# Performance work log

Hardware: AMD Instinct MI355X
Metric: run time of the kernel (lower is better)

## Reference

```python
import jax, jax.numpy as jnp
import numpy as np

D, ED, N, R, K, NL = 128, 256, 16, 8, 4, 3   # d_model, d_inner, d_state, dt_rank, d_conv, n_layers
B, L = 4, 1024
HID, OUT = 256, 2
EPS = 1e-5


def setup_inputs() -> dict:
    key = jax.random.key(0)
    ks = jax.random.split(key, 16)
    g = lambda k, shape, s=0.05: jax.random.normal(k, shape, dtype=jnp.float32) * s
    return {
        "x": jax.random.normal(ks[0], (B, L, D), dtype=jnp.float32),
        # Mamba params, stacked over (2 directions, NL layers)
        "rms_w": jnp.ones((2, NL, D), jnp.float32),
        "in_w": g(ks[1], (2, NL, 2 * ED, D)),
        "in_b": g(ks[2], (2, NL, 2 * ED)),
        "conv_w": g(ks[3], (2, NL, ED, K)),
        "conv_b": g(ks[4], (2, NL, ED)),
        "xproj_w": g(ks[5], (2, NL, R + 2 * N, ED)),
        "dt_w": g(ks[6], (2, NL, ED, R)),
        "dt_b": g(ks[7], (2, NL, ED)),
        "A_log": jnp.broadcast_to(jnp.log(jnp.arange(1.0, N + 1.0, dtype=jnp.float32)), (2, NL, ED, N)) + 0.0,
        "Dp": jnp.ones((2, NL, ED), jnp.float32),
        "out_w": g(ks[8], (2, NL, D, ED)),
        "out_b": g(ks[9], (2, NL, D)),
        # MLP head params (BatchNorm in training mode: batch stats)
        "bn1_g": jnp.ones((2 * D,), jnp.float32), "bn1_b": jnp.zeros((2 * D,), jnp.float32),
        "w1": g(ks[10], (HID, 2 * D)), "b1": g(ks[11], (HID,)),
        "bn2_g": jnp.ones((HID,), jnp.float32), "bn2_b": jnp.zeros((HID,), jnp.float32),
        "w2": g(ks[12], (HID, HID)), "b2": g(ks[13], (HID,)),
        "bn3_g": jnp.ones((HID,), jnp.float32), "bn3_b": jnp.zeros((HID,), jnp.float32),
        "w3": g(ks[14], (OUT, HID)), "b3": g(ks[15], (OUT,)),
    }


def _rms(x, w):
    return x * jax.lax.rsqrt(jnp.mean(x * x, axis=-1, keepdims=True) + EPS) * w


def _dwconv(x, w, b):
    # causal depthwise conv; x: (B,L,ED), w: (ED,K)
    y = jax.lax.conv_general_dilated(x.transpose(0, 2, 1), w[:, None, :], (1,), [(K - 1, 0)],
                                     feature_group_count=ED, dimension_numbers=("NCH", "OIH", "NCH"))
    return y.transpose(0, 2, 1) + b


def _ssm(dA, dBx, C):
    # dA,dBx: (B,L,ED,N); C: (B,L,N) -> y: (B,L,ED)
    def step(h, inp):
        a, bx, c = inp
        h = a * h + bx
        return h, jnp.einsum("ben,bn->be", h, c)
    h0 = jnp.zeros((dA.shape[0], ED, N), dA.dtype)
    _, ys = jax.lax.scan(step, h0, (dA.transpose(1, 0, 2, 3), dBx.transpose(1, 0, 2, 3), C.transpose(1, 0, 2)))
    return ys.transpose(1, 0, 2)


def _block(x, in_w, in_b, conv_w, conv_b, xproj_w, dt_w, dt_b, A_log, Dp, out_w, out_b):
    xz = x @ in_w.T + in_b
    xi, z = xz[..., :ED], xz[..., ED:]
    xi = jax.nn.silu(_dwconv(xi, conv_w, conv_b))
    dbc = xi @ xproj_w.T
    dt, Bm, Cm = dbc[..., :R], dbc[..., R:R + N], dbc[..., R + N:]
    delta = jax.nn.softplus(dt @ dt_w.T + dt_b)            # (B,L,ED)
    A = -jnp.exp(A_log)                                    # (ED,N)
    dA = jnp.exp(delta[..., None] * A)                     # (B,L,ED,N)
    dBx = (delta * xi)[..., None] * Bm[:, :, None, :]      # (B,L,ED,N)
    y = _ssm(dA, dBx, Cm) + Dp * xi
    y = y * jax.nn.silu(z)
    return y @ out_w.T + out_b


def _mamba(x, d, rms_w, in_w, in_b, conv_w, conv_b, xproj_w, dt_w, dt_b, A_log, Dp, out_w, out_b):
    for l in range(NL):
        x = x + _block(_rms(x, rms_w[d, l]), in_w[d, l], in_b[d, l], conv_w[d, l], conv_b[d, l],
                       xproj_w[d, l], dt_w[d, l], dt_b[d, l], A_log[d, l], Dp[d, l], out_w[d, l], out_b[d, l])
    return x


def _bn(x, g, b):
    m = jnp.mean(x, axis=0)
    v = jnp.mean((x - m) ** 2, axis=0)  # biased var, torch BN training mode
    return (x - m) * jax.lax.rsqrt(v + EPS) * g + b


def _forward(x, rms_w, in_w, in_b, conv_w, conv_b, xproj_w, dt_w, dt_b, A_log, Dp, out_w, out_b,
             bn1_g, bn1_b, w1, b1, bn2_g, bn2_b, w2, b2, bn3_g, bn3_b, w3, b3):
    mp = (rms_w, in_w, in_b, conv_w, conv_b, xproj_w, dt_w, dt_b, A_log, Dp, out_w, out_b)
    fwd = _mamba(x, 0, *mp)
    bwd = jnp.flip(_mamba(jnp.flip(x, axis=1), 1, *mp), axis=1)
    h = jnp.concatenate([fwd, bwd], axis=2).reshape(B * L, 2 * D)
    h = jax.nn.leaky_relu(_bn(h, bn1_g, bn1_b) @ w1.T + b1)
    h = jax.nn.leaky_relu(_bn(h, bn2_g, bn2_b) @ w2.T + b2)
    h = _bn(h, bn3_g, bn3_b) @ w3.T + b3
    return h.reshape(B, L, OUT)


def reference(x, rms_w, in_w, in_b, conv_w, conv_b, xproj_w, dt_w, dt_b, A_log, Dp, out_w, out_b,
              bn1_g, bn1_b, w1, b1, bn2_g, bn2_b, w2, b2, bn3_g, bn3_b, w3, b3):
    return _forward(x, rms_w, in_w, in_b, conv_w, conv_b, xproj_w, dt_w, dt_b, A_log, Dp, out_w, out_b,
                    bn1_g, bn1_b, w1, b1, bn2_g, bn2_b, w2, b2, bn3_g, bn3_b, w3, b3)
```

## Files before the change

### kernel.cpp

```cpp
#include <hip/hip_runtime.h>
#include <hip/hip_bf16.h>
#include <hip/hip_fp16.h>

#define NL 3
#define EPS 1e-5f

#define C_INB    393984L
#define C_CONVW  397056L
#define C_CONVB  403200L
#define C_XPROJW 404736L
#define C_DTW    466176L
#define C_DTB    478464L
#define C_ALOG   480000L
#define C_DP     504576L
#define C_OUTB   702720L
#define C_BN1G   703488L
#define C_BN1B   703744L
#define C_B1     769536L
#define C_BN2G   769792L
#define C_BN2B   770048L
#define C_B2     835840L
#define C_BN3G   836096L
#define C_BN3B   836352L
#define C_W3     836608L
#define C_B3     837120L
#define FLAG_OFF 837184L
#define X0_OFF   837248L
#define X1_OFF   1361536L
#define XZT_OFF  1885824L
#define DBCT_OFF 8177280L
#define YGP_OFF  8504960L
#define BNA_OFF  10603648L
#define HINW_OFF  10605184L
#define HOUTW_OFF 10801792L
#define HW1_OFF   10900096L
#define HW2_OFF   10932864L
#define H1_OFF   XZT_OFF
#define H2_OFF   (XZT_OFF + 1048576L)

#define ASLD 68

struct Ptrs { const void* p[25]; };

typedef _Float16 half8 __attribute__((ext_vector_type(8)));
typedef float f32x4 __attribute__((ext_vector_type(4)));

static __device__ const int  CV_SRC[21] = {0,0,3,4,5,6,7,8,9,10,12,13,14,16,17,18,20,21,22,23,24};
static __device__ const long CV_DST[21] = {X0_OFF,X1_OFF,C_INB,C_CONVW,C_CONVB,C_XPROJW,C_DTW,C_DTB,C_ALOG,C_DP,
                                           C_OUTB,C_BN1G,C_BN1B,C_B1,C_BN2G,C_BN2B,C_B2,C_BN3G,C_BN3B,C_W3,C_B3};
static __device__ const int  CV_SZ[21]  = {524288,524288,3072,6144,1536,61440,12288,1536,24576,1536,
                                           768,256,256,256,256,256,256,256,256,512,2};

__device__ inline float ldsrc(const void* s, long i, bool isbf) {
  if (isbf) { unsigned int u = ((const unsigned short*)s)[i]; return __uint_as_float(u << 16); }
  return ((const float*)s)[i];
}

__global__ __launch_bounds__(256) void g_convert(Ptrs ps, float* __restrict__ ws) {
  bool isbf = (*(const unsigned int*)ps.p[1]) == 0x3F803F80u;
  int job = blockIdx.y;
  if (job == 0 && blockIdx.x == 0 && threadIdx.x == 0) ws[FLAG_OFF] = isbf ? 1.f : 0.f;
  int tid0 = blockIdx.x * 256 + threadIdx.x;
  int stride = gridDim.x * 256;
  if (job < 21) {
    int n = CV_SZ[job];
    const void* s = ps.p[CV_SRC[job]];
    float* dp = ws + CV_DST[job];
    bool permute = (job < 2);
    for (int i = tid0; i < n; i += stride) {
      long si = i;
      if (permute) {
        int row = i >> 7, col = i & 127;
        int b = row >> 10, p = row & 1023;
        int t = ((p & 63) << 4) + (p >> 6);
        si = ((long)((b << 10) + t) << 7) + col;
      }
      dp[i] = ldsrc(s, si, isbf);
    }
  } else if (job == 21) {
    _Float16* dp = (_Float16*)(ws + HINW_OFF);
    const void* sw = ps.p[2]; const void* sr = ps.p[1];
    for (int i = tid0; i < 393216; i += stride) {
      int dl = i >> 16, k = i & 127;
      float v = ldsrc(sw, i, isbf) * ldsrc(sr, dl*128 + k, isbf);
      dp[i] = (_Float16)v;
    }
  } else if (job == 22) {
    _Float16* dp = (_Float16*)(ws + HOUTW_OFF);
    const void* s = ps.p[11];
    for (int i = tid0; i < 196608; i += stride) dp[i] = (_Float16)ldsrc(s, i, isbf);
  } else if (job == 23) {
    _Float16* dp = (_Float16*)(ws + HW1_OFF);
    const void* s = ps.p[15];
    for (int i = tid0; i < 65536; i += stride) dp[i] = (_Float16)ldsrc(s, i, isbf);
  } else if (job == 24) {
    _Float16* dp = (_Float16*)(ws + HW2_OFF);
    const void* s = ps.p[19];
    for (int i = tid0; i < 65536; i += stride) dp[i] = (_Float16)ldsrc(s, i, isbf);
  } else {
    for (int i = tid0; i < 1536; i += stride) ws[BNA_OFF + i] = 0.f;
  }
}

__device__ inline void mm_inner(const float* As, const float* Bs, float4* acc) {
  int tx = threadIdx.x & 15, ty = threadIdx.x >> 4;
  #pragma unroll
  for (int k = 0; k < 64; ++k) {
    float4 av = *(const float4*)&As[k*ASLD + ty*4];
    float4 bv = *(const float4*)&Bs[k*ASLD + tx*4];
    acc[0].x = fmaf(av.x,bv.x,acc[0].x); acc[0].y = fmaf(av.x,bv.y,acc[0].y); acc[0].z = fmaf(av.x,bv.z,acc[0].z); acc[0].w = fmaf(av.x,bv.w,acc[0].w);
    acc[1].x = fmaf(av.y,bv.x,acc[1].x); acc[1].y = fmaf(av.y,bv.y,acc[1].y); acc[1].z = fmaf(av.y,bv.z,acc[1].z); acc[1].w = fmaf(av.y,bv.w,acc[1].w);
    acc[2].x = fmaf(av.z,bv.x,acc[2].x); acc[2].y = fmaf(av.z,bv.y,acc[2].y); acc[2].z = fmaf(av.z,bv.z,acc[2].z); acc[2].w = fmaf(av.z,bv.w,acc[2].w);
    acc[3].x = fmaf(av.w,bv.x,acc[3].x); acc[3].y = fmaf(av.w,bv.y,acc[3].y); acc[3].z = fmaf(av.w,bv.z,acc[3].z); acc[3].w = fmaf(av.w,bv.w,acc[3].w);
  }
}

__device__ inline void stageT_g(float* S, const float* src, int ld, int row0, int k0, int nvalid) {
  int m = threadIdx.x >> 2, q = threadIdx.x & 3;
  const float* p = src + (long)(row0 + m) * ld + k0 + q*16;
  bool ok = (row0 + m) < nvalid;
  #pragma unroll
  for (int j = 0; j < 4; ++j) {
    float4 v = ok ? *(const float4*)(p + j*4) : make_float4(0.f,0.f,0.f,0.f);
    int kk = q*16 + j*4;
    S[(kk+0)*ASLD+m] = v.x; S[(kk+1)*ASLD+m] = v.y; S[(kk+2)*ASLD+m] = v.z; S[(kk+3)*ASLD+m] = v.w;
  }
}

__device__ inline float softplusf(float x) {
  if (x > 20.f) return x;
  return __logf(1.f + __expf(x));
}
__device__ inline float siluf(float a) { return a / (1.f + __expf(-a)); }

__global__ __launch_bounds__(256) void g_k1m(float* __restrict__ ws, int layer) {
  int d = blockIdx.z, nt = blockIdx.y, pt = blockIdx.x;
  const float* X = ws + (d ? X1_OFF : X0_OFF);
  const _Float16* Wf = (const _Float16*)(ws + HINW_OFF) + (long)(d*NL+layer)*65536;
  const float* Bi = ws + C_INB + (d*NL+layer)*512;
  __shared__ float rsq[256];
  __shared__ float rsc[64];
  int p0 = pt*64;
  {
    int row = threadIdx.x >> 2, q = threadIdx.x & 3;
    const float* xp = X + (long)(p0+row)*128 + q*32;
    float s = 0.f;
    #pragma unroll
    for (int j = 0; j < 8; ++j) {
      float4 v = *(const float4*)(xp + j*4);
      s += v.x*v.x + v.y*v.y + v.z*v.z + v.w*v.w;
    }
    rsq[row*4+q] = s;
  }
  __syncthreads();
  if (threadIdx.x < 64) {
    float s = rsq[threadIdx.x*4] + rsq[threadIdx.x*4+1] + rsq[threadIdx.x*4+2] + rsq[threadIdx.x*4+3];
    rsc[threadIdx.x] = rsqrtf(s * (1.f/128.f) + EPS);
  }
  __syncthreads();
  int w = threadIdx.x >> 6, lane = threadIdx.x & 63;
  int quad = lane >> 4, lm = lane & 15;
  int n0 = nt*64 + w*16;
  f32x4 zero = {0.f,0.f,0.f,0.f};
  f32x4 acc[4] = {zero, zero, zero, zero};
  #pragma unroll
  for (int s = 0; s < 4; ++s) {
    int k0 = s*32 + quad*8;
    half8 af = *(const half8*)(Wf + (long)(n0+lm)*128 + k0);
    #pragma unroll
    for (int t = 0; t < 4; ++t) {
      int pr = t*16 + lm;
      const float* xp = X + (long)(p0+pr)*128 + k0;
      float4 v0 = *(const float4*)xp;
      float4 v1 = *(const float4*)(xp+4);
      float r = rsc[pr];
      half8 bf;
      bf[0]=(_Float16)(v0.x*r); bf[1]=(_Float16)(v0.y*r); bf[2]=(_Float16)(v0.z*r); bf[3]=(_Float16)(v0.w*r);
      bf[4]=(_Float16)(v1.x*r); bf[5]=(_Float16)(v1.y*r); bf[6]=(_Float16)(v1.z*r); bf[7]=(_Float16)(v1.w*r);
      acc[t] = __builtin_amdgcn_mfma_f32_16x16x32_f16(af, bf, acc[t], 0, 0, 0);
    }
  }
  float* xzt = ws + XZT_OFF + (long)d*2097152L;
  #pragma unroll
  for (int r = 0; r < 4; ++r) {
    int n = n0 + quad*4 + r;
    float bias = Bi[n];
    #pragma unroll
    for (int t = 0; t < 4; ++t) {
      int p = p0 + t*16 + lm;
      xzt[(long)n*4096 + p] = acc[t][r] + bias;
    }
  }
}

__global__ __launch_bounds__(256) void g_k3c(float* __restrict__ ws, int layer) {
  int d = blockIdx.z, mt = blockIdx.x;
  int m0 = mt * 64;
  int bb = mt >> 4, ii = mt & 15;
  const float* xzbase = ws + XZT_OFF + (long)d*2097152L;
  const float* W = ws + C_XPROJW + (long)((d*NL+layer)*40) * 256;
  const float* cw = ws + C_CONVW + (long)(d*NL+layer)*1024;
  const float* cbp = ws + C_CONVB + (d*NL+layer)*256;
  __shared__ float As[64*ASLD];
  __shared__ float Bs[64*ASLD];
  int colb[4]; int edge[4];
  #pragma unroll
  for (int j = 0; j < 4; ++j) {
    if (d == 0) {
      int iq = ii - j;
      if (iq >= 0) { colb[j] = iq*64; edge[j] = 0; }
      else         { colb[j] = (iq+16)*64 - 1; edge[j] = 1; }
    } else {
      int iq = ii + j;
      if (iq <= 15) { colb[j] = iq*64; edge[j] = 0; }
      else          { colb[j] = (iq-16)*64 + 1; edge[j] = 2; }
    }
  }
  int m = threadIdx.x & 63, er = threadIdx.x >> 6;
  float4 acc[4] = {make_float4(0,0,0,0),make_float4(0,0,0,0),make_float4(0,0,0,0),make_float4(0,0,0,0)};
  for (int kt = 0; kt < 4; ++kt) {
    for (int pass = 0; pass < 16; ++pass) {
      int el = pass*4 + er;
      int e = kt*64 + el;
      const float* xr = xzbase + (long)e*4096 + bb*1024;
      float4 cwv = *(const float4*)(cw + e*4);
      float cb = cbp[e];
      float xv[4];
      #pragma unroll
      for (int j = 0; j < 4; ++j) {
        bool msk = (edge[j] == 1 && m == 0) || (edge[j] == 2 && m == 63);
        xv[j] = msk ? 0.f : xr[colb[j] + m];
      }
      float a = cb + cwv.w*xv[0] + cwv.z*xv[1] + cwv.y*xv[2] + cwv.x*xv[3];
      As[el*ASLD + m] = siluf(a);
    }
    stageT_g(Bs, W, 256, 0, kt*64, 40);
    __syncthreads();
    mm_inner(As, Bs, acc);
    __syncthreads();
  }
  int tx = threadIdx.x & 15, ty = threadIdx.x >> 4;
  #pragma unroll
  for (int i = 0; i < 4; ++i) {
    const float* av = (const float*)&acc[i];
    #pragma unroll
    for (int cc = 0; cc < 4; ++cc) {
      Bs[(tx*4+cc)*65 + ty*4+i] = av[cc];
    }
  }
  __syncthreads();
  float* dbcT = ws + DBCT_OFF + (long)d*163840L;
  #pragma unroll
  for (int r = 0; r < 10; ++r) {
    int el = r*256 + threadIdx.x;
    int n = el >> 6, mm = el & 63;
    dbcT[(long)n*4096 + m0 + mm] = Bs[n*65 + mm];
  }
}

__global__ __launch_bounds__(256) void g_k5c(float* __restrict__ ws, int layer) {
  int d = blockIdx.z, b = blockIdx.y, eg = blockIdx.x;
  int es = threadIdx.x >> 6;
  int c  = threadIdx.x & 63;
  int e = eg*4 + es;
  int g0 = b*1024 + c;
  const float* xzrow = ws + XZT_OFF + (long)d*2097152L + (long)e*4096 + g0;
  const float* zp    = ws + XZT_OFF + (long)d*2097152L + (long)(256+e)*4096 + g0;
  const float* dbc = ws + DBCT_OFF + (long)d*163840L + g0;
  float*       yo  = ws + YGP_OFF + (long)d*1048576L + (long)e*4096 + g0;
  const float* dw = ws + C_DTW + (long)((d*NL+layer)*256 + e)*8;
  float dtb = ws[C_DTB + (d*NL+layer)*256 + e];
  const float* al = ws + C_ALOG + (long)((d*NL+layer)*256 + e)*16;
  float Dpe = ws[C_DP + (d*NL+layer)*256 + e];
  float4 cwv = *(const float4*)(ws + C_CONVW + (long)((d*NL+layer)*256 + e)*4);
  float cb = ws[C_CONVB + (d*NL+layer)*256 + e];
  float dtw[8];
  #pragma unroll
  for (int n = 0; n < 8; ++n) dtw[n] = dw[n];
  float Anv[16]; bool fast = true;
  #pragma unroll
  for (int n = 0; n < 16; ++n) {
    Anv[n] = -__expf(al[n]);
    fast = fast && (fabsf(Anv[n] + (float)(n+1)) < 1e-3f * (float)(n+1));
  }
  float w1, w2, w3;
  if (d == 0) {
    if (c > 0) { w1 = xzrow[959]; w2 = xzrow[895]; w3 = xzrow[831]; }
    else { w1 = w2 = w3 = 0.f; }
  } else {
    if (c < 63) { w1 = xzrow[1]; w2 = xzrow[65]; w3 = xzrow[129]; }
    else { w1 = w2 = w3 = 0.f; }
  }
  __shared__ float aL[4*64*17];
  __shared__ float hL[4*64*17];
  float h[16], ap[16], del[16], xcv[16];
  float Q = 1.f;
  #pragma unroll
  for (int n = 0; n < 16; ++n) { h[n] = 0.f; ap[n] = 1.f; }
  int i0 = d ? 15 : 0, di = d ? -1 : 1;
  for (int s = 0; s < 16; ++s) {
    int i = i0 + s*di;
    int off = i*64;
    float a0 = dtb;
    #pragma unroll
    for (int n = 0; n < 8; ++n) a0 += dbc[(long)n*4096 + off] * dtw[n];
    float dl = softplusf(a0);
    float xt = xzrow[off];
    float xc = siluf(cb + cwv.w*xt + cwv.z*w1 + cwv.y*w2 + cwv.x*w3);
    w3 = w2; w2 = w1; w1 = xt;
    del[s] = dl; xcv[s] = xc;
    float dx = dl * xc;
    if (fast) {
      float q = __expf(-dl);
      float qp[16];
      qp[0]=q; qp[1]=q*q; qp[2]=qp[1]*q; qp[3]=qp[1]*qp[1];
      float q4=qp[3];
      qp[4]=qp[0]*q4; qp[5]=qp[1]*q4; qp[6]=qp[2]*q4; qp[7]=q4*q4;
      float q8=qp[7];
      #pragma unroll
      for (int j = 0; j < 8; ++j) qp[8+j]=qp[j]*q8;
      Q *= q;
      #pragma unroll
      for (int n = 0; n < 16; ++n)
        h[n] = fmaf(qp[n], h[n], dx * dbc[(long)(8+n)*4096 + off]);
    } else {
      #pragma unroll
      for (int n = 0; n < 16; ++n) {
        float a = __expf(dl * Anv[n]);
        ap[n] *= a;
        h[n] = fmaf(a, h[n], dx * dbc[(long)(8+n)*4096 + off]);
      }
    }
  }
  if (fast) {
    float p = Q;
    #pragma unroll
    for (int n = 0; n < 16; ++n) { ap[n] = p; p *= Q; }
  }
  int base = (es*64 + c)*17;
  #pragma unroll
  for (int n = 0; n < 16; ++n) { aL[base+n] = ap[n]; hL[base+n] = h[n]; }
  __syncthreads();
  if (threadIdx.x < 64) {
    int e2 = threadIdx.x >> 4, n = threadIdx.x & 15;
    float h0 = 0.f;
    for (int s2 = 0; s2 < 64; ++s2) {
      int cc = d ? (63 - s2) : s2;
      int ix = (e2*64 + cc)*17 + n;
      float ta = aL[ix], th = hL[ix];
      aL[ix] = h0;
      h0 = fmaf(ta, h0, th);
    }
  }
  __syncthreads();
  #pragma unroll
  for (int n = 0; n < 16; ++n) h[n] = aL[base+n];
  for (int s = 0; s < 16; ++s) {
    int i = i0 + s*di;
    int off = i*64;
    float dl = del[s], xc = xcv[s];
    float dx = dl * xc;
    float zr = zp[off];
    float zg = zr / (1.f + __expf(-zr));
    float ya[4] = {0.f,0.f,0.f,0.f};
    if (fast) {
      float q = __expf(-dl);
      float qp[16];
      qp[0]=q; qp[1]=q*q; qp[2]=qp[1]*q; qp[3]=qp[1]*qp[1];
      float q4=qp[3];
      qp[4]=qp[0]*q4; qp[5]=qp[1]*q4; qp[6]=qp[2]*q4; qp[7]=q4*q4;
      float q8=qp[7];
      #pragma unroll
      for (int j = 0; j < 8; ++j) qp[8+j]=qp[j]*q8;
      #pragma unroll
      for (int n = 0; n < 16; ++n) {
        h[n] = fmaf(qp[n], h[n], dx * dbc[(long)(8+n)*4096 + off]);
        ya[n & 3] = fmaf(h[n], dbc[(long)(24+n)*4096 + off], ya[n & 3]);
      }
    } else {
      #pragma unroll
      for (int n = 0; n < 16; ++n) {
        float a = __expf(dl * Anv[n]);
        h[n] = fmaf(a, h[n], dx * dbc[(long)(8+n)*4096 + off]);
        ya[n & 3] = fmaf(h[n], dbc[(long)(24+n)*4096 + off], ya[n & 3]);
      }
    }
    float y = (ya[0] + ya[1]) + (ya[2] + ya[3]);
    y = fmaf(Dpe, xc, y);
    yo[off] = y * zg;
  }
}

__global__ __launch_bounds__(256) void g_k61(float* __restrict__ ws, int layer) {
  int d = blockIdx.z, pt = blockIdx.x;
  int p0 = pt*16;
  const float* Y = ws + YGP_OFF + (long)d*1048576L;
  const _Float16* Wf = (const _Float16*)(ws + HOUTW_OFF) + (long)(d*NL+layer)*32768;
  const float* Ob = ws + C_OUTB + (d*NL+layer)*128;
  float* Xd = ws + (d ? X1_OFF : X0_OFF);
  __shared__ __align__(16) _Float16 Ah[16*264];
  __shared__ float Xn[16*137];
  __shared__ float rsq[64];
  __shared__ float rsc[16];
  {
    int e = threadIdx.x;
    const float* yp = Y + (long)e*4096 + p0;
    float4 v0 = *(const float4*)yp;
    float4 v1 = *(const float4*)(yp+4);
    float4 v2 = *(const float4*)(yp+8);
    float4 v3 = *(const float4*)(yp+12);
    float vv[16] = {v0.x,v0.y,v0.z,v0.w, v1.x,v1.y,v1.z,v1.w,
                    v2.x,v2.y,v2.z,v2.w, v3.x,v3.y,v3.z,v3.w};
    #pragma unroll
    for (int p = 0; p < 16; ++p) Ah[p*264 + e] = (_Float16)vv[p];
  }
  __syncthreads();
  int w = threadIdx.x >> 6, lane = threadIdx.x & 63;
  int quad = lane >> 4, lm = lane & 15;
  f32x4 zero = {0.f,0.f,0.f,0.f};
  f32x4 acc[2] = {zero, zero};
  #pragma unroll
  for (int s = 0; s < 8; ++s) {
    int k0 = s*32 + quad*8;
    half8 af = *(const half8*)(&Ah[lm*264 + k0]);
    #pragma unroll
    for (int t = 0; t < 2; ++t) {
      int n = w*32 + t*16 + lm;
      half8 bf = *(const half8*)(Wf + (long)n*256 + k0);
      acc[t] = __builtin_amdgcn_mfma_f32_16x16x32_f16(af, bf, acc[t], 0, 0, 0);
    }
  }
  bool dostats = (layer == NL-1);
  float* bna = ws + BNA_OFF;
  #pragma unroll
  for (int t = 0; t < 2; ++t) {
    int n = w*32 + t*16 + lm;
    float ob = Ob[n];
    float s1 = 0.f, s2 = 0.f;
    #pragma unroll
    for (int r = 0; r < 4; ++r) {
      int p = p0 + quad*4 + r;
      float v = acc[t][r] + ob + Xd[(long)p*128 + n];
      Xd[(long)p*128 + n] = v;
      Xn[(quad*4 + r)*137 + n] = v;
      s1 += v; s2 += v*v;
    }
    if (dostats) {
      s1 += __shfl_xor(s1, 16, 64); s2 += __shfl_xor(s2, 16, 64);
      s1 += __shfl_xor(s1, 32, 64); s2 += __shfl_xor(s2, 32, 64);
      if (quad == 0) {
        int ch = d*128 + n;
        atomicAdd(&bna[ch], s1);
        atomicAdd(&bna[256 + ch], s2);
      }
    }
  }
  if (layer == NL-1) return;
  __syncthreads();
  if (threadIdx.x < 64) {
    int pl = threadIdx.x >> 2, qq = threadIdx.x & 3;
    float s = 0.f;
    const float* xr = &Xn[pl*137 + qq*32];
    #pragma unroll
    for (int k = 0; k < 32; ++k) s += xr[k]*xr[k];
    rsq[threadIdx.x] = s;
  }
  __syncthreads();
  if (threadIdx.x < 16) {
    float s = rsq[threadIdx.x*4] + rsq[threadIdx.x*4+1] + rsq[threadIdx.x*4+2] + rsq[threadIdx.x*4+3];
    rsc[threadIdx.x] = rsqrtf(s * (1.f/128.f) + EPS);
  }
  __syncthreads();
  const _Float16* Wn = (const _Float16*)(ws + HINW_OFF) + (long)(d*NL+layer+1)*65536;
  const float* Bi = ws + C_INB + (d*NL+layer+1)*512;
  f32x4 acc2[8] = {zero,zero,zero,zero,zero,zero,zero,zero};
  float r = rsc[lm];
  #pragma unroll
  for (int s = 0; s < 4; ++s) {
    int k0 = s*32 + quad*8;
    half8 bf;
    const float* xr = &Xn[lm*137 + k0];
    #pragma unroll
    for (int j = 0; j < 8; ++j) bf[j] = (_Float16)(xr[j] * r);
    #pragma unroll
    for (int tt = 0; tt < 8; ++tt) {
      int n2 = w*128 + tt*16 + lm;
      half8 af = *(const half8*)(Wn + (long)n2*128 + k0);
      acc2[tt] = __builtin_amdgcn_mfma_f32_16x16x32_f16(af, bf, acc2[tt], 0, 0, 0);
    }
  }
  float* xzt = ws + XZT_OFF + (long)d*2097152L;
  #pragma unroll
  for (int tt = 0; tt < 8; ++tt) {
    #pragma unroll
    for (int rr = 0; rr < 4; ++rr) {
      int n2 = w*128 + tt*16 + quad*4 + rr;
      xzt[(long)n2*4096 + p0 + lm] = acc2[tt][rr] + Bi[n2];
    }
  }
}

template<int STAGE>
__global__ __launch_bounds__(256) void g_hgm(float* __restrict__ ws) {
  int p0 = blockIdx.x * 16;
  __shared__ float scL[256], shL[256];
  {
    int k = threadIdx.x;
    float S = ws[BNA_OFF + STAGE*512 + k], S2 = ws[BNA_OFF + STAGE*512 + 256 + k];
    float mean = S * (1.f/4096.f);
    float var = S2 * (1.f/4096.f) - mean*mean;
    const float* g = ws + (STAGE == 0 ? C_BN1G : C_BN2G);
    const float* bb = ws + (STAGE == 0 ? C_BN1B : C_BN2B);
    float sc = g[k] * rsqrtf(var + EPS);
    scL[k] = sc; shL[k] = bb[k] - mean*sc;
  }
  __syncthreads();
  const _Float16* Wf = (const _Float16*)(ws + (STAGE == 0 ? HW1_OFF : HW2_OFF));
  const float* bias = ws + (STAGE == 0 ? C_B1 : C_B2);
  float* H = ws + (STAGE == 0 ? H1_OFF : H2_OFF);
  int w = threadIdx.x >> 6, lane = threadIdx.x & 63;
  int quad = lane >> 4, lm = lane & 15;
  f32x4 zero = {0.f,0.f,0.f,0.f};
  f32x4 acc[4] = {zero, zero, zero, zero};
  #pragma unroll
  for (int s = 0; s < 8; ++s) {
    int k0 = s*32 + quad*8;
    const float* src;
    if (STAGE == 0) src = (k0 < 128) ? (ws + X0_OFF + (long)(p0+lm)*128 + k0)
                                     : (ws + X1_OFF + (long)(p0+lm)*128 + (k0-128));
    else            src = ws + H1_OFF + (long)(p0+lm)*256 + k0;
    float4 v0 = *(const float4*)src, v1 = *(const float4*)(src+4);
    float4 c0 = *(const float4*)&scL[k0], c1 = *(const float4*)&scL[k0+4];
    float4 h0 = *(const float4*)&shL[k0], h1 = *(const float4*)&shL[k0+4];
    half8 af;
    af[0]=(_Float16)(v0.x*c0.x+h0.x); af[1]=(_Float16)(v0.y*c0.y+h0.y);
    af[2]=(_Float16)(v0.z*c0.z+h0.z); af[3]=(_Float16)(v0.w*c0.w+h0.w);
    af[4]=(_Float16)(v1.x*c1.x+h1.x); af[5]=(_Float16)(v1.y*c1.y+h1.y);
    af[6]=(_Float16)(v1.z*c1.z+h1.z); af[7]=(_Float16)(v1.w*c1.w+h1.w);
    #pragma unroll
    for (int t = 0; t < 4; ++t) {
      int n = w*64 + t*16 + lm;
      half8 bf = *(const half8*)(Wf + (long)n*256 + k0);
      acc[t] = __builtin_amdgcn_mfma_f32_16x16x32_f16(af, bf, acc[t], 0, 0, 0);
    }
  }
  float* bna = ws + BNA_OFF + (STAGE+1)*512;
  #pragma unroll
  for (int t = 0; t < 4; ++t) {
    int n = w*64 + t*16 + lm;
    float bs = bias[n];
    float s1 = 0.f, s2 = 0.f;
    #pragma unroll
    for (int r = 0; r < 4; ++r) {
      int p = p0 + quad*4 + r;
      float v = acc[t][r] + bs;
      v = v > 0.f ? v : 0.01f*v;
      H[(long)p*256 + n] = v;
      s1 += v; s2 += v*v;
    }
    s1 += __shfl_xor(s1, 16, 64); s2 += __shfl_xor(s2, 16, 64);
    s1 += __shfl_xor(s1, 32, 64); s2 += __shfl_xor(s2, 32, 64);
    if (quad == 0) {
      atomicAdd(&bna[n], s1);
      atomicAdd(&bna[256 + n], s2);
    }
  }
}

__global__ __launch_bounds__(256) void g_hg2(float* __restrict__ ws, void* dout) {
  int mt = blockIdx.x;
  __shared__ float As[64*ASLD];
  __shared__ float Bs[64*ASLD];
  __shared__ float scL[256], shL[256];
  {
    int k = threadIdx.x;
    float S = ws[BNA_OFF + 2*512 + k], S2 = ws[BNA_OFF + 2*512 + 256 + k];
    float mean = S * (1.f/4096.f);
    float var = S2 * (1.f/4096.f) - mean*mean;
    float sc = ws[C_BN3G + k] * rsqrtf(var + EPS);
    scL[k] = sc; shL[k] = ws[C_BN3B + k] - mean*sc;
  }
  __syncthreads();
  float4 acc[4] = {make_float4(0,0,0,0),make_float4(0,0,0,0),make_float4(0,0,0,0),make_float4(0,0,0,0)};
  for (int kt = 0; kt < 4; ++kt) {
    int k0 = kt * 64;
    {
      int m = threadIdx.x >> 2, q = threadIdx.x & 3;
      const float* p = ws + H2_OFF + (long)(mt*64 + m)*256 + k0 + q*16;
      #pragma unroll
      for (int j = 0; j < 4; ++j) {
        float4 v  = *(const float4*)(p + j*4);
        float4 s4 = *(const float4*)&scL[k0 + q*16 + j*4];
        float4 h4 = *(const float4*)&shL[k0 + q*16 + j*4];
        int kk = q*16 + j*4;
        As[(kk+0)*ASLD+m] = v.x*s4.x + h4.x; As[(kk+1)*ASLD+m] = v.y*s4.y + h4.y;
        As[(kk+2)*ASLD+m] = v.z*s4.z + h4.z; As[(kk+3)*ASLD+m] = v.w*s4.w + h4.w;
      }
    }
    stageT_g(Bs, ws + C_W3, 256, 0, k0, 2);
    __syncthreads();
    mm_inner(As, Bs, acc);
    __syncthreads();
  }
  int tx = threadIdx.x & 15, ty = threadIdx.x >> 4;
  if (tx == 0) {
    bool isbf = ws[FLAG_OFF] != 0.f;
    float b0 = ws[C_B3], b1 = ws[C_B3 + 1];
    #pragma unroll
    for (int i = 0; i < 4; ++i) {
      int r = mt*64 + ty*4 + i;
      int b = r >> 10, p = r & 1023;
      int t = ((p & 63) << 4) + (p >> 6);
      long tok = (long)(b << 10) + t;
      float v0 = acc[i].x + b0, v1 = acc[i].y + b1;
      if (isbf) {
        __hip_bfloat16* o = (__hip_bfloat16*)dout;
        o[tok*2]   = __float2bfloat16(v0);
        o[tok*2+1] = __float2bfloat16(v1);
      } else {
        float* o = (float*)dout;
        o[tok*2] = v0; o[tok*2+1] = v1;
      }
    }
  }
}

extern "C" void kernel_launch(void* const* d_in, const int* in_sizes, int n_in,
                              void* d_out, int out_size, void* d_ws, size_t ws_size,
                              hipStream_t stream) {
  (void)in_sizes; (void)n_in; (void)out_size; (void)ws_size;
  float* ws = (float*)d_ws;
  Ptrs ps;
  for (int i = 0; i < 25; ++i) ps.p[i] = d_in[i];
  g_convert<<<dim3(32, 26), dim3(256), 0, stream>>>(ps, ws);
  g_k1m<<<dim3(64, 8, 2), dim3(256), 0, stream>>>(ws, 0);
  for (int l = 0; l < NL; ++l) {
    g_k3c<<<dim3(64, 1, 2), dim3(256), 0, stream>>>(ws, l);
    g_k5c<<<dim3(64, 4, 2), dim3(256), 0, stream>>>(ws, l);
    g_k61<<<dim3(256, 1, 2), dim3(256), 0, stream>>>(ws, l);
  }
  g_hgm<0><<<dim3(256), dim3(256), 0, stream>>>(ws);
  g_hgm<1><<<dim3(256), dim3(256), 0, stream>>>(ws);
  g_hg2<<<dim3(64), dim3(256), 0, stream>>>(ws, d_out);
}
```

Baseline: 468.7 us.

## Use fp16 MFMA for conv+x_proj kernel with pre-converted padded weights

Replaces the fp32 SIMT-tiled conv+SiLU+x_proj kernel with one that stages the activated conv output as fp16 in shared memory and multiplies it against fp16 x_proj weights using 16x16x32 MFMA instructions. The weights are converted once in the setup kernel, padded from 40 to 64 rows and stored in a new workspace region. The grid moves from 128 blocks of 64 tokens to 256 blocks of 32 tokens. The aim is to cut FMA time and raise parallelism, at the cost of fp16 rounding on the x_proj inputs and some wasted work on the padded rows.

Result: faster. 405.2 us (-13.6%).

```diff
diff --git a/kernel.cpp b/kernel.cpp
--- a/kernel.cpp
+++ b/kernel.cpp
@@ -35,6 +35,7 @@
 #define HOUTW_OFF 10801792L
 #define HW1_OFF   10900096L
 #define HW2_OFF   10932864L
+#define HXW_OFF   10965632L
 #define H1_OFF   XZT_OFF
 #define H2_OFF   (XZT_OFF + 1048576L)
 
@@ -97,8 +98,18 @@
     _Float16* dp = (_Float16*)(ws + HW2_OFF);
     const void* s = ps.p[19];
     for (int i = tid0; i < 65536; i += stride) dp[i] = (_Float16)ldsrc(s, i, isbf);
+  } else if (job == 25) {
+    for (int i = tid0; i < 1536; i += stride) ws[BNA_OFF + i] = 0.f;
   } else {
-    for (int i = tid0; i < 1536; i += stride) ws[BNA_OFF + i] = 0.f;
+    _Float16* dp = (_Float16*)(ws + HXW_OFF);
+    const void* s = ps.p[5];
+    for (int i = tid0; i < 98304; i += stride) {
+      int dl = i >> 14;
+      int rem = i & 16383;
+      int nn = rem >> 8, k = rem & 255;
+      float v = (nn < 40) ? ldsrc(s, (long)(dl*40+nn)*256 + k, isbf) : 0.f;
+      dp[i] = (_Float16)v;
+    }
   }
 }
 
@@ -193,68 +204,70 @@
   }
 }
 
-__global__ __launch_bounds__(256) void g_k3c(float* __restrict__ ws, int layer) {
-  int d = blockIdx.z, mt = blockIdx.x;
-  int m0 = mt * 64;
-  int bb = mt >> 4, ii = mt & 15;
-  const float* xzbase = ws + XZT_OFF + (long)d*2097152L;
-  const float* W = ws + C_XPROJW + (long)((d*NL+layer)*40) * 256;
+#define AHLD 264
+__global__ __launch_bounds__(256) void g_k3m(float* __restrict__ ws, int layer) {
+  int d = blockIdx.z, b = blockIdx.y;
+  int ii = blockIdx.x >> 1, c0 = (blockIdx.x & 1) * 32;
+  const float* xz = ws + XZT_OFF + (long)d*2097152L;
   const float* cw = ws + C_CONVW + (long)(d*NL+layer)*1024;
   const float* cbp = ws + C_CONVB + (d*NL+layer)*256;
-  __shared__ float As[64*ASLD];
-  __shared__ float Bs[64*ASLD];
-  int colb[4]; int edge[4];
-  #pragma unroll
-  for (int j = 0; j < 4; ++j) {
-    if (d == 0) {
-      int iq = ii - j;
-      if (iq >= 0) { colb[j] = iq*64; edge[j] = 0; }
-      else         { colb[j] = (iq+16)*64 - 1; edge[j] = 1; }
-    } else {
-      int iq = ii + j;
-      if (iq <= 15) { colb[j] = iq*64; edge[j] = 0; }
-      else          { colb[j] = (iq-16)*64 + 1; edge[j] = 2; }
-    }
-  }
-  int m = threadIdx.x & 63, er = threadIdx.x >> 6;
-  float4 acc[4] = {make_float4(0,0,0,0),make_float4(0,0,0,0),make_float4(0,0,0,0),make_float4(0,0,0,0)};
-  for (int kt = 0; kt < 4; ++kt) {
-    for (int pass = 0; pass < 16; ++pass) {
-      int el = pass*4 + er;
-      int e = kt*64 + el;
-      const float* xr = xzbase + (long)e*4096 + bb*1024;
-      float4 cwv = *(const float4*)(cw + e*4);
-      float cb = cbp[e];
-      float xv[4];
-      #pragma unroll
-      for (int j = 0; j < 4; ++j) {
-        bool msk = (edge[j] == 1 && m == 0) || (edge[j] == 2 && m == 63);
-        xv[j] = msk ? 0.f : xr[colb[j] + m];
-      }
-      float a = cb + cwv.w*xv[0] + cwv.z*xv[1] + cwv.y*xv[2] + cwv.x*xv[3];
-      As[el*ASLD + m] = siluf(a);
-    }
-    stageT_g(Bs, W, 256, 0, kt*64, 40);
-    __syncthreads();
-    mm_inner(As, Bs, acc);
-    __syncthreads();
-  }
-  int tx = threadIdx.x & 15, ty = threadIdx.x >> 4;
-  #pragma unroll
-  for (int i = 0; i < 4; ++i) {
-    const float* av = (const float*)&acc[i];
-    #pragma unroll
-    for (int cc = 0; cc < 4; ++cc) {
-      Bs[(tx*4+cc)*65 + ty*4+i] = av[cc];
-    }
-  }
-  __syncthreads();
+  const _Float16* Wx = (const _Float16*)(ws + HXW_OFF) + (long)(d*NL+layer)*16384;
+  __shared__ __align__(16) _Float16 Ah[32*AHLD];
+  int col[4], sh[4];
+  col[0] = ii; sh[0] = 0;
+  #pragma unroll
+  for (int j = 1; j < 4; ++j) {
+    if (d == 0) { if (ii-j >= 0) { col[j]=ii-j; sh[j]=0; } else { col[j]=ii-j+16; sh[j]=-1; } }
+    else        { if (ii+j <= 15){ col[j]=ii+j; sh[j]=0; } else { col[j]=ii+j-16; sh[j]=1; } }
+  }
+  int c = threadIdx.x & 31, eh = threadIdx.x >> 5;
+  int gc = c0 + c;
+  long rowbase = (long)b*1024;
+  for (int r = 0; r < 32; ++r) {
+    int e = eh*32 + r;
+    const float* xrow = xz + (long)e*4096 + rowbase;
+    float4 cwv = *(const float4*)(cw + e*4);
+    float v0 = xrow[col[0]*64 + gc];
+    float v1, v2, v3;
+    {
+      bool bad = (sh[1] < 0 && gc == 0) || (sh[1] > 0 && gc == 63);
+      v1 = bad ? 0.f : xrow[col[1]*64 + gc + sh[1]];
+    }
+    {
+      bool bad = (sh[2] < 0 && gc == 0) || (sh[2] > 0 && gc == 63);
+      v2 = bad ? 0.f : xrow[col[2]*64 + gc + sh[2]];
+    }
+    {
+      bool bad = (sh[3] < 0 && gc == 0) || (sh[3] > 0 && gc == 63);
+      v3 = bad ? 0.f : xrow[col[3]*64 + gc + sh[3]];
+    }
+    float a = cbp[e] + cwv.w*v0 + cwv.z*v1 + cwv.y*v2 + cwv.x*v3;
+    Ah[c*AHLD + e] = (_Float16)siluf(a);
+  }
+  __syncthreads();
+  int w = threadIdx.x >> 6, lane = threadIdx.x & 63;
+  int quad = lane >> 4, lm = lane & 15;
+  f32x4 zero = {0.f,0.f,0.f,0.f};
+  f32x4 acc[2] = {zero, zero};
+  #pragma unroll
+  for (int s = 0; s < 8; ++s) {
+    int k0 = s*32 + quad*8;
+    half8 af = *(const half8*)(Wx + (long)(w*16+lm)*256 + k0);
+    #pragma unroll
+    for (int t = 0; t < 2; ++t) {
+      half8 bf = *(const half8*)(&Ah[(t*16+lm)*AHLD + k0]);
+      acc[t] = __builtin_amdgcn_mfma_f32_16x16x32_f16(af, bf, acc[t], 0, 0, 0);
+    }
+  }
   float* dbcT = ws + DBCT_OFF + (long)d*163840L;
-  #pragma unroll
-  for (int r = 0; r < 10; ++r) {
-    int el = r*256 + threadIdx.x;
-    int n = el >> 6, mm = el & 63;
-    dbcT[(long)n*4096 + m0 + mm] = Bs[n*65 + mm];
+  long P0 = (long)b*1024 + ii*64 + c0;
+  #pragma unroll
+  for (int t = 0; t < 2; ++t) {
+    #pragma unroll
+    for (int r = 0; r < 4; ++r) {
+      int n = w*16 + quad*4 + r;
+      if (n < 40) dbcT[(long)n*4096 + P0 + t*16 + lm] = acc[t][r];
+    }
   }
 }
 
@@ -632,10 +645,10 @@
   float* ws = (float*)d_ws;
   Ptrs ps;
   for (int i = 0; i < 25; ++i) ps.p[i] = d_in[i];
-  g_convert<<<dim3(32, 26), dim3(256), 0, stream>>>(ps, ws);
+  g_convert<<<dim3(32, 27), dim3(256), 0, stream>>>(ps, ws);
   g_k1m<<<dim3(64, 8, 2), dim3(256), 0, stream>>>(ws, 0);
   for (int l = 0; l < NL; ++l) {
-    g_k3c<<<dim3(64, 1, 2), dim3(256), 0, stream>>>(ws, l);
+    g_k3m<<<dim3(32, 4, 2), dim3(256), 0, stream>>>(ws, l);
     g_k5c<<<dim3(64, 4, 2), dim3(256), 0, stream>>>(ws, l);
     g_k61<<<dim3(256, 1, 2), dim3(256), 0, stream>>>(ws, l);
   }
```
